# Kernel optimization log

Hardware: AMD Instinct MI355X
Metric: run time of the kernel (lower is better)

## Reference

```python
import jax, jax.numpy as jnp
import numpy as np

IN_CH = 32
OUT_CH = 32
B, N = 1, 100000
E = 1600000
BN_EPS = 1e-5


def setup_inputs() -> dict:
    key = jax.random.key(0)
    k1, k2, k3 = jax.random.split(key, 3)
    x = jax.random.normal(k1, (B, IN_CH, N, 1), dtype=jnp.float32)
    edge_index = jax.random.randint(k2, (2, E), 0, B * N, dtype=jnp.int64)
    # Conv1d(in*2 -> out, kernel_size=1, bias=False): weight [out, 2*in]
    W = jax.random.normal(k3, (OUT_CH, 2 * IN_CH), dtype=jnp.float32) * (1.0 / np.sqrt(2 * IN_CH))
    gamma = jnp.ones((OUT_CH,), dtype=jnp.float32)
    beta = jnp.zeros((OUT_CH,), dtype=jnp.float32)
    return {"x": x, "edge_index": edge_index, "W": W, "gamma": gamma, "beta": beta}


def reference(x, edge_index, W, gamma, beta):
    Bb, C, Nn, _ = x.shape
    out_ch = W.shape[0]
    # faithful to torch: x.squeeze(-1).view(B*N, C) (raw row-major reshape)
    x_flat = x[..., 0].reshape(Bb * Nn, C)
    src, tgt = edge_index[0], edge_index[1]
    x_s = x_flat[src]                      # [E, C] gather
    x_t = x_flat[tgt]                      # [E, C] gather
    ef = jnp.concatenate([x_s, x_t - x_s], axis=1)  # [E, 2C]
    y = ef @ W.T                           # 1x1 conv == GEMM, [E, out]
    # BatchNorm1d in training mode: batch stats over edge dim (biased var)
    mean = jnp.mean(y, axis=0)
    var = jnp.mean(jnp.square(y - mean), axis=0)
    y = (y - mean) * jax.lax.rsqrt(var + BN_EPS) * gamma + beta
    # ELU (alpha=1)
    y = jnp.where(y > 0, y, jnp.expm1(y))
    out = jnp.zeros((Bb * Nn, out_ch), dtype=y.dtype).at[src].add(y)  # scatter-add
    return out.reshape(Bb, out_ch, Nn)[..., None]
```

## Files before the change

kernel.cpp:

```cpp
#include <hip/hip_runtime.h>
#include <hip/hip_bf16.h>
#include <math.h>

#define NCH 32

typedef unsigned short ushort_t;
typedef unsigned int uint_t;
typedef unsigned char uchar_t;

static __device__ __forceinline__ float bf2f(ushort_t b) {
    return __uint_as_float(((uint_t)b) << 16);
}
static __device__ __forceinline__ ushort_t f2bf(float f) {
    __hip_bfloat16 h = __float2bfloat16(f);
    return *reinterpret_cast<ushort_t*>(&h);
}

using f32x2 = __attribute__((ext_vector_type(2))) float;

template <typename T>
__device__ __forceinline__ auto pkAddImpl(T* p, T v, int)
    -> decltype(unsafeAtomicAdd(p, v), void()) {
    unsafeAtomicAdd(p, v);
}
template <typename T>
__device__ void pkAddImpl(T* p, T v, long) {
    uint_t* q = reinterpret_cast<uint_t*>(p);
    uint_t vv = *reinterpret_cast<uint_t*>(&v);
    uint_t cur = *q;
    while (true) {
        float lo = bf2f((ushort_t)(cur & 0xFFFF)) + bf2f((ushort_t)(vv & 0xFFFF));
        float hi = bf2f((ushort_t)(cur >> 16)) + bf2f((ushort_t)(vv >> 16));
        uint_t nw = (uint_t)f2bf(lo) | ((uint_t)f2bf(hi) << 16);
        uint_t prev = atomicCAS(q, cur, nw);
        if (prev == cur) break;
        cur = prev;
    }
}
static __device__ __forceinline__ void pkAdd(__hip_bfloat162* p, float z0, float z1) {
    __hip_bfloat162 v;
    v.x = __float2bfloat16(z0);
    v.y = __float2bfloat16(z1);
    pkAddImpl(p, v, 0);
}


__global__ __launch_bounds__(256) void k_uv3(
    const float* __restrict__ x, const float* __restrict__ W,
    ushort_t* __restrict__ uh, ushort_t* __restrict__ vh,
    uchar_t* __restrict__ uq, uchar_t* __restrict__ vq, int N)
{
    __shared__ float At[NCH * NCH];
    __shared__ float Bt[NCH * NCH];
    for (int i = threadIdx.x; i < NCH * NCH; i += 256) {
        const int k = i >> 5, c = i & 31;
        const float w1 = W[c * 64 + k];
        const float w2 = W[c * 64 + 32 + k];
        At[i] = w1 - w2;
        Bt[i] = w2;
    }
    __syncthreads();

    const int n = blockIdx.x * 8 + (threadIdx.x >> 5);
    const int c = threadIdx.x & 31;
    if (n >= N) return;

    const float xc = x[(size_t)n * NCH + c];
    float su = 0.f, sv = 0.f;
#pragma unroll
    for (int k = 0; k < NCH; ++k) {
        const float xk = __shfl(xc, k, 32);
        su = fmaf(At[k * 32 + c], xk, su);
        sv = fmaf(Bt[k * 32 + c], xk, sv);
    }
    uh[(size_t)n * NCH + c] = f2bf(su);
    vh[(size_t)n * NCH + c] = f2bf(sv);
    uq[(size_t)n * NCH + c] =
        (uchar_t)(__builtin_amdgcn_cvt_pk_fp8_f32(su, su, 0, false) & 0xFF);
    vq[(size_t)n * NCH + c] =
        (uchar_t)(__builtin_amdgcn_cvt_pk_fp8_f32(sv, sv, 0, false) & 0xFF);
}

__global__ __launch_bounds__(256) void k_stats8(
    const uchar_t* __restrict__ uq, const uchar_t* __restrict__ vq,
    const int* __restrict__ srci, const int* __restrict__ tgti,
    float* __restrict__ partials, int E)
{
    const ushort_t* __restrict__ uq16 = (const ushort_t*)uq;
    const ushort_t* __restrict__ vq16 = (const ushort_t*)vq;
    const int l  = threadIdx.x & 15;
    const int g  = (blockIdx.x * 256 + threadIdx.x) >> 4;
    const int nG = (gridDim.x * 256) >> 4;

    float s0 = 0.f, s1 = 0.f, q0 = 0.f, q1 = 0.f;
    int e = g;
    for (; e + 3 * nG < E; e += 4 * nG) {
        const int ea = e, eb = e + nG, ec = e + 2 * nG, ed = e + 3 * nG;
        const int sa = srci[ea], sb = srci[eb], sc = srci[ec], sd = srci[ed];
        const int ta = tgti[ea], tb = tgti[eb], tc = tgti[ec], td = tgti[ed];
        const ushort_t ua = uq16[(size_t)sa * 16 + l];
        const ushort_t ub = uq16[(size_t)sb * 16 + l];
        const ushort_t uc = uq16[(size_t)sc * 16 + l];
        const ushort_t ud = uq16[(size_t)sd * 16 + l];
        const ushort_t va = vq16[(size_t)ta * 16 + l];
        const ushort_t vb = vq16[(size_t)tb * 16 + l];
        const ushort_t vc = vq16[(size_t)tc * 16 + l];
        const ushort_t vd = vq16[(size_t)td * 16 + l];
#pragma unroll
        for (int k = 0; k < 4; ++k) {
            const ushort_t uu = (k == 0) ? ua : (k == 1) ? ub : (k == 2) ? uc : ud;
            const ushort_t vv = (k == 0) ? va : (k == 1) ? vb : (k == 2) ? vc : vd;
            const f32x2 uf = __builtin_amdgcn_cvt_pk_f32_fp8((int)uu, false);
            const f32x2 vf = __builtin_amdgcn_cvt_pk_f32_fp8((int)vv, false);
            const float y0 = uf.x + vf.x;
            const float y1 = uf.y + vf.y;
            s0 += y0; q0 = fmaf(y0, y0, q0);
            s1 += y1; q1 = fmaf(y1, y1, q1);
        }
    }
    for (; e < E; e += nG) {
        const int s = srci[e], t = tgti[e];
        const f32x2 uf = __builtin_amdgcn_cvt_pk_f32_fp8((int)uq16[(size_t)s * 16 + l], false);
        const f32x2 vf = __builtin_amdgcn_cvt_pk_f32_fp8((int)vq16[(size_t)t * 16 + l], false);
        const float y0 = uf.x + vf.x;
        const float y1 = uf.y + vf.y;
        s0 += y0; q0 = fmaf(y0, y0, q0);
        s1 += y1; q1 = fmaf(y1, y1, q1);
    }

    __shared__ float sL[16][32];
    __shared__ float qL[16][32];
    const int grp = threadIdx.x >> 4;
    sL[grp][2 * l + 0] = s0;
    sL[grp][2 * l + 1] = s1;
    qL[grp][2 * l + 0] = q0;
    qL[grp][2 * l + 1] = q1;
    __syncthreads();
    if (threadIdx.x < 32) {
        float a = 0.f;
#pragma unroll
        for (int r = 0; r < 16; ++r) a += sL[r][threadIdx.x];
        partials[(size_t)blockIdx.x * 64 + threadIdx.x] = a;
    } else if (threadIdx.x < 64) {
        const int cc = threadIdx.x - 32;
        float a = 0.f;
#pragma unroll
        for (int r = 0; r < 16; ++r) a += qL[r][cc];
        partials[(size_t)blockIdx.x * 64 + 32 + cc] = a;
    }
}

__global__ __launch_bounds__(256) void k_finalize(
    const float* __restrict__ partials, int nblocks,
    const float* __restrict__ gamma, const float* __restrict__ beta,
    float* __restrict__ ab, float invE)
{
    __shared__ float acc[4][64];
    const int vtx = threadIdx.x & 63, chunk = threadIdx.x >> 6;
    float s = 0.f;
    for (int r = chunk; r < nblocks; r += 4) s += partials[(size_t)r * 64 + vtx];
    acc[chunk][vtx] = s;
    __syncthreads();
    if (threadIdx.x < 64) acc[0][vtx] = acc[0][vtx] + acc[1][vtx] + acc[2][vtx] + acc[3][vtx];
    __syncthreads();
    if (threadIdx.x < 32) {
        const int c = threadIdx.x;
        float mean = acc[0][c] * invE;
        float var  = acc[0][32 + c] * invE - mean * mean;
        float rstd = rsqrtf(var + 1e-5f);
        float a = gamma[c] * rstd;
        ab[c] = a; ab[32 + c] = beta[c] - mean * a;
    }
}

__global__ __launch_bounds__(256) void k_apply_pk(
    const ushort_t* __restrict__ uh, const ushort_t* __restrict__ vh,
    const int* __restrict__ srci, const int* __restrict__ tgti,
    const float* __restrict__ ab,
    __hip_bfloat162* __restrict__ outh, int E)
{
    const uint_t* __restrict__ uh32 = (const uint_t*)uh;
    const uint_t* __restrict__ vh32 = (const uint_t*)vh;
    const int l  = threadIdx.x & 15;
    const float a0 = ab[2 * l + 0], a1 = ab[2 * l + 1];
    const float b0 = ab[32 + 2 * l + 0], b1 = ab[32 + 2 * l + 1];
    const int g  = (blockIdx.x * 256 + threadIdx.x) >> 4;
    const int nG = (gridDim.x * 256) >> 4;

    int e = g;
    for (; e + 3 * nG < E; e += 4 * nG) {
        const int ea = e, eb = e + nG, ec = e + 2 * nG, ed = e + 3 * nG;
        const int sa = srci[ea], sb = srci[eb], sc = srci[ec], sd = srci[ed];
        const int ta = tgti[ea], tb = tgti[eb], tc = tgti[ec], td = tgti[ed];
        const uint_t Ua = uh32[(size_t)sa * 16 + l];
        const uint_t Ub = uh32[(size_t)sb * 16 + l];
        const uint_t Uc = uh32[(size_t)sc * 16 + l];
        const uint_t Ud = uh32[(size_t)sd * 16 + l];
        const uint_t Va = vh32[(size_t)ta * 16 + l];
        const uint_t Vb = vh32[(size_t)tb * 16 + l];
        const uint_t Vc = vh32[(size_t)tc * 16 + l];
        const uint_t Vd = vh32[(size_t)td * 16 + l];
        const int ss[4] = {sa, sb, sc, sd};
        const uint_t UU[4] = {Ua, Ub, Uc, Ud};
        const uint_t VV[4] = {Va, Vb, Vc, Vd};
#pragma unroll
        for (int k = 0; k < 4; ++k) {
            const float y0 = bf2f((ushort_t)(UU[k] & 0xFFFF)) + bf2f((ushort_t)(VV[k] & 0xFFFF));
            const float y1 = bf2f((ushort_t)(UU[k] >> 16))    + bf2f((ushort_t)(VV[k] >> 16));
            float z0 = fmaf(a0, y0, b0);
            float z1 = fmaf(a1, y1, b1);
            z0 = (z0 > 0.f) ? z0 : (__expf(z0) - 1.0f);
            z1 = (z1 > 0.f) ? z1 : (__expf(z1) - 1.0f);
            pkAdd(&outh[(size_t)ss[k] * 16 + l], z0, z1);
        }
    }
    for (; e < E; e += nG) {
        const int s = srci[e], t = tgti[e];
        const uint_t U = uh32[(size_t)s * 16 + l];
        const uint_t V = vh32[(size_t)t * 16 + l];
        const float y0 = bf2f((ushort_t)(U & 0xFFFF)) + bf2f((ushort_t)(V & 0xFFFF));
        const float y1 = bf2f((ushort_t)(U >> 16))    + bf2f((ushort_t)(V >> 16));
        float z0 = fmaf(a0, y0, b0);
        float z1 = fmaf(a1, y1, b1);
        z0 = (z0 > 0.f) ? z0 : (__expf(z0) - 1.0f);
        z1 = (z1 > 0.f) ? z1 : (__expf(z1) - 1.0f);
        pkAdd(&outh[(size_t)s * 16 + l], z0, z1);
    }
}

__global__ __launch_bounds__(256) void k_cvt(
    const uint_t* __restrict__ outh32, float* __restrict__ out, int M)
{
    const int i = blockIdx.x * 256 + threadIdx.x;
    if (i >= M) return;
    const uint_t w = outh32[i];
    float2 f;
    f.x = bf2f((ushort_t)(w & 0xFFFF));
    f.y = bf2f((ushort_t)(w >> 16));
    ((float2*)out)[i] = f;
}

__global__ __launch_bounds__(256) void k_stats_hist(
    const float* __restrict__ x,
    const int* __restrict__ srci, const int* __restrict__ tgti,
    const float* __restrict__ W,
    float* __restrict__ partials, int E)
{
    float sum[NCH], ssq[NCH];
#pragma unroll
    for (int c = 0; c < NCH; ++c) { sum[c] = 0.f; ssq[c] = 0.f; }
    const int stride = gridDim.x * blockDim.x;
    for (int e = blockIdx.x * blockDim.x + threadIdx.x; e < E; e += stride) {
        const int s = srci[e], t = tgti[e];
        const float4* ps = (const float4*)(x + (size_t)s * NCH);
        const float4* pt = (const float4*)(x + (size_t)t * NCH);
        float xs[NCH], dx[NCH];
#pragma unroll
        for (int i = 0; i < 8; ++i) {
            float4 a = ps[i], bb = pt[i];
            xs[4*i+0] = a.x; xs[4*i+1] = a.y; xs[4*i+2] = a.z; xs[4*i+3] = a.w;
            dx[4*i+0] = bb.x - a.x; dx[4*i+1] = bb.y - a.y;
            dx[4*i+2] = bb.z - a.z; dx[4*i+3] = bb.w - a.w;
        }
#pragma unroll
        for (int c = 0; c < NCH; ++c) {
            const float* wr = W + c * 64;
            float y = 0.f;
#pragma unroll
            for (int k = 0; k < NCH; ++k) y = fmaf(wr[k], xs[k], y);
#pragma unroll
            for (int k = 0; k < NCH; ++k) y = fmaf(wr[32 + k], dx[k], y);
            sum[c] += y;
            ssq[c] = fmaf(y, y, ssq[c]);
        }
    }
#pragma unroll
    for (int c = 0; c < NCH; ++c) {
#pragma unroll
        for (int off = 32; off > 0; off >>= 1) {
            sum[c] += __shfl_down(sum[c], off);
            ssq[c] += __shfl_down(ssq[c], off);
        }
    }
    __shared__ float red[4][64];
    const int lane = threadIdx.x & 63, wave = threadIdx.x >> 6;
    if (lane == 0) {
#pragma unroll
        for (int c = 0; c < NCH; ++c) { red[wave][c] = sum[c]; red[wave][NCH+c] = ssq[c]; }
    }
    __syncthreads();
    if (threadIdx.x < 64)
        partials[(size_t)blockIdx.x * 64 + threadIdx.x] =
            red[0][threadIdx.x] + red[1][threadIdx.x] + red[2][threadIdx.x] + red[3][threadIdx.x];
}

__global__ __launch_bounds__(256) void k_apply_atomic(
    const float* __restrict__ x,
    const int* __restrict__ srci, const int* __restrict__ tgti,
    const float* __restrict__ W, const float* __restrict__ ab,
    float* __restrict__ out, int E)
{
    const int e = blockIdx.x * 256 + threadIdx.x;
    if (e >= E) return;
    const int s = srci[e], t = tgti[e];
    const float4* ps = (const float4*)(x + (size_t)s * NCH);
    const float4* pt = (const float4*)(x + (size_t)t * NCH);
    float xs[NCH], dx[NCH];
#pragma unroll
    for (int i = 0; i < 8; ++i) {
        float4 a = ps[i], bb = pt[i];
        xs[4*i+0] = a.x; xs[4*i+1] = a.y; xs[4*i+2] = a.z; xs[4*i+3] = a.w;
        dx[4*i+0] = bb.x - a.x; dx[4*i+1] = bb.y - a.y;
        dx[4*i+2] = bb.z - a.z; dx[4*i+3] = bb.w - a.w;
    }
    float* orow = out + (size_t)s * NCH;
#pragma unroll
    for (int c = 0; c < NCH; ++c) {
        const float* wr = W + c * 64;
        float y = 0.f;
#pragma unroll
        for (int k = 0; k < NCH; ++k) y = fmaf(wr[k], xs[k], y);
#pragma unroll
        for (int k = 0; k < NCH; ++k) y = fmaf(wr[32 + k], dx[k], y);
        float z = fmaf(ab[c], y, ab[32 + c]);
        z = (z > 0.f) ? z : (__expf(z) - 1.0f);
        atomicAdd(orow + c, z);
    }
}

extern "C" void kernel_launch(void* const* d_in, const int* in_sizes, int n_in,
                              void* d_out, int out_size, void* d_ws, size_t ws_size,
                              hipStream_t stream)
{
    const float* x     = (const float*)d_in[0];
    const int*   ei    = (const int*)d_in[1];
    const float* W     = (const float*)d_in[2];
    const float* gamma = (const float*)d_in[3];
    const float* beta  = (const float*)d_in[4];
    const int E = in_sizes[1] / 2;
    const int N = in_sizes[0] / NCH;
    const int* srci = ei;
    const int* tgti = ei + E;

    const int SB = 1024;
    const int AB = 2048;

    size_t need = (size_t)N * NCH * (2 + 2 + 1 + 1 + 2)
                + ((size_t)SB * 64 + 64) * 4;

    if (ws_size >= need) {
        ushort_t* uh      = (ushort_t*)d_ws;
        ushort_t* vh      = uh + (size_t)N * NCH;
        uchar_t*  uq      = (uchar_t*)(vh + (size_t)N * NCH);
        uchar_t*  vq      = uq + (size_t)N * NCH;
        __hip_bfloat162* outh = (__hip_bfloat162*)(vq + (size_t)N * NCH);
        float*    partials= (float*)((ushort_t*)outh + (size_t)N * NCH);
        float*    ab      = partials + (size_t)SB * 64;

        hipMemsetAsync(outh, 0, (size_t)N * NCH * 2, stream);
        k_uv3<<<(N + 7) / 8, 256, 0, stream>>>(x, W, uh, vh, uq, vq, N);
        k_stats8<<<SB, 256, 0, stream>>>(uq, vq, srci, tgti, partials, E);
        k_finalize<<<1, 256, 0, stream>>>(partials, SB, gamma, beta, ab, 1.0f / (float)E);
        k_apply_pk<<<AB, 256, 0, stream>>>(uh, vh, srci, tgti, ab, outh, E);
        k_cvt<<<(N * 16 + 255) / 256, 256, 0, stream>>>((const uint_t*)outh,
                                                        (float*)d_out, N * 16);
    } else {
        const int SBf = 512;
        float* ab       = (float*)d_ws;
        float* partials = ab + 64;
        hipMemsetAsync(d_out, 0, (size_t)out_size * sizeof(float), stream);
        k_stats_hist<<<SBf, 256, 0, stream>>>(x, srci, tgti, W, partials, E);
        k_finalize<<<1, 256, 0, stream>>>(partials, SBf, gamma, beta, ab, 1.0f / (float)E);
        k_apply_atomic<<<(E + 255) / 256, 256, 0, stream>>>(x, srci, tgti, W, ab,
                                                            (float*)d_out, E);
    }
}
```

Before: 309.3 us.

## Partition scatter by source range per XCD and fuse memset/finalize into kernels

The output zeroing moves into the projection kernel and the BN finalize becomes a last-block-ticket epilogue of the stats kernel, which removes a memset and a kernel launch. The apply kernel now gives each group of blocks (blockIdx & 7, meant to map to one XCD) one eighth of the source-node range. Each group scans all edges and processes only those whose source falls in its range, so the atomics on each output slice stay within one L2. The cost is that every edge index is read eight times, and the grid-stride work per group shrinks to one eighth of the blocks.

Result: slower. 501.1 us (+62.0%).

```diff
diff --git a/kernel.cpp b/kernel.cpp
--- a/kernel.cpp
+++ b/kernel.cpp
@@ -45,10 +45,11 @@
 }
 
 
-__global__ __launch_bounds__(256) void k_uv3(
+__global__ __launch_bounds__(256) void k_uv3z(
     const float* __restrict__ x, const float* __restrict__ W,
     ushort_t* __restrict__ uh, ushort_t* __restrict__ vh,
-    uchar_t* __restrict__ uq, uchar_t* __restrict__ vq, int N)
+    uchar_t* __restrict__ uq, uchar_t* __restrict__ vq,
+    uint_t* __restrict__ outh32, int* __restrict__ ticket, int N)
 {
     __shared__ float At[NCH * NCH];
     __shared__ float Bt[NCH * NCH];
@@ -59,12 +60,18 @@
         At[i] = w1 - w2;
         Bt[i] = w2;
     }
+
+    {
+        const int M = N * 16;
+        for (int i = blockIdx.x * 256 + threadIdx.x; i < M; i += gridDim.x * 256)
+            outh32[i] = 0u;
+        if (blockIdx.x == 0 && threadIdx.x == 0) *ticket = 0;
+    }
     __syncthreads();
 
     const int n = blockIdx.x * 8 + (threadIdx.x >> 5);
     const int c = threadIdx.x & 31;
     if (n >= N) return;
-
     const float xc = x[(size_t)n * NCH + c];
     float su = 0.f, sv = 0.f;
 #pragma unroll
@@ -81,10 +88,12 @@
         (uchar_t)(__builtin_amdgcn_cvt_pk_fp8_f32(sv, sv, 0, false) & 0xFF);
 }
 
-__global__ __launch_bounds__(256) void k_stats8(
+__global__ __launch_bounds__(256) void k_stats8f(
     const uchar_t* __restrict__ uq, const uchar_t* __restrict__ vq,
     const int* __restrict__ srci, const int* __restrict__ tgti,
-    float* __restrict__ partials, int E)
+    float* __restrict__ partials, int* __restrict__ ticket,
+    const float* __restrict__ gamma, const float* __restrict__ beta,
+    float* __restrict__ ab, float invE, int E)
 {
     const ushort_t* __restrict__ uq16 = (const ushort_t*)uq;
     const ushort_t* __restrict__ vq16 = (const ushort_t*)vq;
@@ -148,6 +157,189 @@
         for (int r = 0; r < 16; ++r) a += qL[r][cc];
         partials[(size_t)blockIdx.x * 64 + 32 + cc] = a;
     }
+
+    __shared__ int isLast;
+    __threadfence();
+    __syncthreads();
+    if (threadIdx.x == 0) {
+        const int prev = atomicAdd(ticket, 1);
+        isLast = (prev == (int)gridDim.x - 1) ? 1 : 0;
+    }
+    __syncthreads();
+    if (isLast) {
+        __shared__ float acc[4][64];
+        const int vtx = threadIdx.x & 63, chunk = threadIdx.x >> 6;
+        float s = 0.f;
+        for (int r = chunk; r < (int)gridDim.x; r += 4)
+            s += partials[(size_t)r * 64 + vtx];
+        acc[chunk][vtx] = s;
+        __syncthreads();
+        if (threadIdx.x < 64)
+            acc[0][vtx] = acc[0][vtx] + acc[1][vtx] + acc[2][vtx] + acc[3][vtx];
+        __syncthreads();
+        if (threadIdx.x < 32) {
+            const int c = threadIdx.x;
+            float mean = acc[0][c] * invE;
+            float var  = acc[0][32 + c] * invE - mean * mean;
+            float rstd = rsqrtf(var + 1e-5f);
+            float a = gamma[c] * rstd;
+            ab[c] = a; ab[32 + c] = beta[c] - mean * a;
+        }
+    }
+}
+
+__global__ __launch_bounds__(256) void k_apply_xcd(
+    const ushort_t* __restrict__ uh, const ushort_t* __restrict__ vh,
+    const int* __restrict__ srci, const int* __restrict__ tgti,
+    const float* __restrict__ ab,
+    __hip_bfloat162* __restrict__ outh, int E, int NS)
+{
+    const uint_t* __restrict__ uh32 = (const uint_t*)uh;
+    const uint_t* __restrict__ vh32 = (const uint_t*)vh;
+    const int l  = threadIdx.x & 15;
+    const float a0 = ab[2 * l + 0], a1 = ab[2 * l + 1];
+    const float b0 = ab[32 + 2 * l + 0], b1 = ab[32 + 2 * l + 1];
+
+    const int xb = blockIdx.x & 7;
+    const int lo = xb * NS;
+    const int bi = blockIdx.x >> 3;
+    const int nb = gridDim.x >> 3;
+    const int g  = (bi * 256 + threadIdx.x) >> 4;
+    const int nG = nb * 16;
+
+    int e = g;
+    for (; e + 3 * nG < E; e += 4 * nG) {
+        const int ea = e, eb = e + nG, ec = e + 2 * nG, ed = e + 3 * nG;
+        const int sa = srci[ea], sb = srci[eb], sc = srci[ec], sd = srci[ed];
+        const bool ma = (unsigned)(sa - lo) < (unsigned)NS;
+        const bool mb = (unsigned)(sb - lo) < (unsigned)NS;
+        const bool mc = (unsigned)(sc - lo) < (unsigned)NS;
+        const bool md = (unsigned)(sd - lo) < (unsigned)NS;
+        if (ma) {
+            const uint_t U = uh32[(size_t)sa * 16 + l];
+            const uint_t V = vh32[(size_t)tgti[ea] * 16 + l];
+            const float y0 = bf2f((ushort_t)(U & 0xFFFF)) + bf2f((ushort_t)(V & 0xFFFF));
+            const float y1 = bf2f((ushort_t)(U >> 16))    + bf2f((ushort_t)(V >> 16));
+            float z0 = fmaf(a0, y0, b0);
+            float z1 = fmaf(a1, y1, b1);
+            z0 = (z0 > 0.f) ? z0 : (__expf(z0) - 1.0f);
+            z1 = (z1 > 0.f) ? z1 : (__expf(z1) - 1.0f);
+            pkAdd(&outh[(size_t)sa * 16 + l], z0, z1);
+        }
+        if (mb) {
+            const uint_t U = uh32[(size_t)sb * 16 + l];
+            const uint_t V = vh32[(size_t)tgti[eb] * 16 + l];
+            const float y0 = bf2f((ushort_t)(U & 0xFFFF)) + bf2f((ushort_t)(V & 0xFFFF));
+            const float y1 = bf2f((ushort_t)(U >> 16))    + bf2f((ushort_t)(V >> 16));
+            float z0 = fmaf(a0, y0, b0);
+            float z1 = fmaf(a1, y1, b1);
+            z0 = (z0 > 0.f) ? z0 : (__expf(z0) - 1.0f);
+            z1 = (z1 > 0.f) ? z1 : (__expf(z1) - 1.0f);
+            pkAdd(&outh[(size_t)sb * 16 + l], z0, z1);
+        }
+        if (mc) {
+            const uint_t U = uh32[(size_t)sc * 16 + l];
+            const uint_t V = vh32[(size_t)tgti[ec] * 16 + l];
+            const float y0 = bf2f((ushort_t)(U & 0xFFFF)) + bf2f((ushort_t)(V & 0xFFFF));
+            const float y1 = bf2f((ushort_t)(U >> 16))    + bf2f((ushort_t)(V >> 16));
+            float z0 = fmaf(a0, y0, b0);
+            float z1 = fmaf(a1, y1, b1);
+            z0 = (z0 > 0.f) ? z0 : (__expf(z0) - 1.0f);
+            z1 = (z1 > 0.f) ? z1 : (__expf(z1) - 1.0f);
+            pkAdd(&outh[(size_t)sc * 16 + l], z0, z1);
+        }
+        if (md) {
+            const uint_t U = uh32[(size_t)sd * 16 + l];
+            const uint_t V = vh32[(size_t)tgti[ed] * 16 + l];
+            const float y0 = bf2f((ushort_t)(U & 0xFFFF)) + bf2f((ushort_t)(V & 0xFFFF));
+            const float y1 = bf2f((ushort_t)(U >> 16))    + bf2f((ushort_t)(V >> 16));
+            float z0 = fmaf(a0, y0, b0);
+            float z1 = fmaf(a1, y1, b1);
+            z0 = (z0 > 0.f) ? z0 : (__expf(z0) - 1.0f);
+            z1 = (z1 > 0.f) ? z1 : (__expf(z1) - 1.0f);
+            pkAdd(&outh[(size_t)sd * 16 + l], z0, z1);
+        }
+    }
+    for (; e < E; e += nG) {
+        const int s = srci[e];
+        if ((unsigned)(s - lo) < (unsigned)NS) {
+            const uint_t U = uh32[(size_t)s * 16 + l];
+            const uint_t V = vh32[(size_t)tgti[e] * 16 + l];
+            const float y0 = bf2f((ushort_t)(U & 0xFFFF)) + bf2f((ushort_t)(V & 0xFFFF));
+            const float y1 = bf2f((ushort_t)(U >> 16))    + bf2f((ushort_t)(V >> 16));
+            float z0 = fmaf(a0, y0, b0);
+            float z1 = fmaf(a1, y1, b1);
+            z0 = (z0 > 0.f) ? z0 : (__expf(z0) - 1.0f);
+            z1 = (z1 > 0.f) ? z1 : (__expf(z1) - 1.0f);
+            pkAdd(&outh[(size_t)s * 16 + l], z0, z1);
+        }
+    }
+}
+
+__global__ __launch_bounds__(256) void k_cvt(
+    const uint_t* __restrict__ outh32, float* __restrict__ out, int M)
+{
+    const int i = blockIdx.x * 256 + threadIdx.x;
+    if (i >= M) return;
+    const uint_t w = outh32[i];
+    float2 f;
+    f.x = bf2f((ushort_t)(w & 0xFFFF));
+    f.y = bf2f((ushort_t)(w >> 16));
+    ((float2*)out)[i] = f;
+}
+
+__global__ __launch_bounds__(256) void k_stats_hist(
+    const float* __restrict__ x,
+    const int* __restrict__ srci, const int* __restrict__ tgti,
+    const float* __restrict__ W,
+    float* __restrict__ partials, int E)
+{
+    float sum[NCH], ssq[NCH];
+#pragma unroll
+    for (int c = 0; c < NCH; ++c) { sum[c] = 0.f; ssq[c] = 0.f; }
+    const int stride = gridDim.x * blockDim.x;
+    for (int e = blockIdx.x * blockDim.x + threadIdx.x; e < E; e += stride) {
+        const int s = srci[e], t = tgti[e];
+        const float4* ps = (const float4*)(x + (size_t)s * NCH);
+        const float4* pt = (const float4*)(x + (size_t)t * NCH);
+        float xs[NCH], dx[NCH];
+#pragma unroll
+        for (int i = 0; i < 8; ++i) {
+            float4 a = ps[i], bb = pt[i];
+            xs[4*i+0] = a.x; xs[4*i+1] = a.y; xs[4*i+2] = a.z; xs[4*i+3] = a.w;
+            dx[4*i+0] = bb.x - a.x; dx[4*i+1] = bb.y - a.y;
+            dx[4*i+2] = bb.z - a.z; dx[4*i+3] = bb.w - a.w;
+        }
+#pragma unroll
+        for (int c = 0; c < NCH; ++c) {
+            const float* wr = W + c * 64;
+            float y = 0.f;
+#pragma unroll
+            for (int k = 0; k < NCH; ++k) y = fmaf(wr[k], xs[k], y);
+#pragma unroll
+            for (int k = 0; k < NCH; ++k) y = fmaf(wr[32 + k], dx[k], y);
+            sum[c] += y;
+            ssq[c] = fmaf(y, y, ssq[c]);
+        }
+    }
+#pragma unroll
+    for (int c = 0; c < NCH; ++c) {
+#pragma unroll
+        for (int off = 32; off > 0; off >>= 1) {
+            sum[c] += __shfl_down(sum[c], off);
+            ssq[c] += __shfl_down(ssq[c], off);
+        }
+    }
+    __shared__ float red[4][64];
+    const int lane = threadIdx.x & 63, wave = threadIdx.x >> 6;
+    if (lane == 0) {
+#pragma unroll
+        for (int c = 0; c < NCH; ++c) { red[wave][c] = sum[c]; red[wave][NCH+c] = ssq[c]; }
+    }
+    __syncthreads();
+    if (threadIdx.x < 64)
+        partials[(size_t)blockIdx.x * 64 + threadIdx.x] =
+            red[0][threadIdx.x] + red[1][threadIdx.x] + red[2][threadIdx.x] + red[3][threadIdx.x];
 }
 
 __global__ __launch_bounds__(256) void k_finalize(
@@ -171,127 +363,6 @@
         float a = gamma[c] * rstd;
         ab[c] = a; ab[32 + c] = beta[c] - mean * a;
     }
-}
-
-__global__ __launch_bounds__(256) void k_apply_pk(
-    const ushort_t* __restrict__ uh, const ushort_t* __restrict__ vh,
-    const int* __restrict__ srci, const int* __restrict__ tgti,
-    const float* __restrict__ ab,
-    __hip_bfloat162* __restrict__ outh, int E)
-{
-    const uint_t* __restrict__ uh32 = (const uint_t*)uh;
-    const uint_t* __restrict__ vh32 = (const uint_t*)vh;
-    const int l  = threadIdx.x & 15;
-    const float a0 = ab[2 * l + 0], a1 = ab[2 * l + 1];
-    const float b0 = ab[32 + 2 * l + 0], b1 = ab[32 + 2 * l + 1];
-    const int g  = (blockIdx.x * 256 + threadIdx.x) >> 4;
-    const int nG = (gridDim.x * 256) >> 4;
-
-    int e = g;
-    for (; e + 3 * nG < E; e += 4 * nG) {
-        const int ea = e, eb = e + nG, ec = e + 2 * nG, ed = e + 3 * nG;
-        const int sa = srci[ea], sb = srci[eb], sc = srci[ec], sd = srci[ed];
-        const int ta = tgti[ea], tb = tgti[eb], tc = tgti[ec], td = tgti[ed];
-        const uint_t Ua = uh32[(size_t)sa * 16 + l];
-        const uint_t Ub = uh32[(size_t)sb * 16 + l];
-        const uint_t Uc = uh32[(size_t)sc * 16 + l];
-        const uint_t Ud = uh32[(size_t)sd * 16 + l];
-        const uint_t Va = vh32[(size_t)ta * 16 + l];
-        const uint_t Vb = vh32[(size_t)tb * 16 + l];
-        const uint_t Vc = vh32[(size_t)tc * 16 + l];
-        const uint_t Vd = vh32[(size_t)td * 16 + l];
-        const int ss[4] = {sa, sb, sc, sd};
-        const uint_t UU[4] = {Ua, Ub, Uc, Ud};
-        const uint_t VV[4] = {Va, Vb, Vc, Vd};
-#pragma unroll
-        for (int k = 0; k < 4; ++k) {
-            const float y0 = bf2f((ushort_t)(UU[k] & 0xFFFF)) + bf2f((ushort_t)(VV[k] & 0xFFFF));
-            const float y1 = bf2f((ushort_t)(UU[k] >> 16))    + bf2f((ushort_t)(VV[k] >> 16));
-            float z0 = fmaf(a0, y0, b0);
-            float z1 = fmaf(a1, y1, b1);
-            z0 = (z0 > 0.f) ? z0 : (__expf(z0) - 1.0f);
-            z1 = (z1 > 0.f) ? z1 : (__expf(z1) - 1.0f);
-            pkAdd(&outh[(size_t)ss[k] * 16 + l], z0, z1);
-        }
-    }
-    for (; e < E; e += nG) {
-        const int s = srci[e], t = tgti[e];
-        const uint_t U = uh32[(size_t)s * 16 + l];
-        const uint_t V = vh32[(size_t)t * 16 + l];
-        const float y0 = bf2f((ushort_t)(U & 0xFFFF)) + bf2f((ushort_t)(V & 0xFFFF));
-        const float y1 = bf2f((ushort_t)(U >> 16))    + bf2f((ushort_t)(V >> 16));
-        float z0 = fmaf(a0, y0, b0);
-        float z1 = fmaf(a1, y1, b1);
-        z0 = (z0 > 0.f) ? z0 : (__expf(z0) - 1.0f);
-        z1 = (z1 > 0.f) ? z1 : (__expf(z1) - 1.0f);
-        pkAdd(&outh[(size_t)s * 16 + l], z0, z1);
-    }
-}
-
-__global__ __launch_bounds__(256) void k_cvt(
-    const uint_t* __restrict__ outh32, float* __restrict__ out, int M)
-{
-    const int i = blockIdx.x * 256 + threadIdx.x;
-    if (i >= M) return;
-    const uint_t w = outh32[i];
-    float2 f;
-    f.x = bf2f((ushort_t)(w & 0xFFFF));
-    f.y = bf2f((ushort_t)(w >> 16));
-    ((float2*)out)[i] = f;
-}
-
-__global__ __launch_bounds__(256) void k_stats_hist(
-    const float* __restrict__ x,
-    const int* __restrict__ srci, const int* __restrict__ tgti,
-    const float* __restrict__ W,
-    float* __restrict__ partials, int E)
-{
-    float sum[NCH], ssq[NCH];
-#pragma unroll
-    for (int c = 0; c < NCH; ++c) { sum[c] = 0.f; ssq[c] = 0.f; }
-    const int stride = gridDim.x * blockDim.x;
-    for (int e = blockIdx.x * blockDim.x + threadIdx.x; e < E; e += stride) {
-        const int s = srci[e], t = tgti[e];
-        const float4* ps = (const float4*)(x + (size_t)s * NCH);
-        const float4* pt = (const float4*)(x + (size_t)t * NCH);
-        float xs[NCH], dx[NCH];
-#pragma unroll
-        for (int i = 0; i < 8; ++i) {
-            float4 a = ps[i], bb = pt[i];
-            xs[4*i+0] = a.x; xs[4*i+1] = a.y; xs[4*i+2] = a.z; xs[4*i+3] = a.w;
-            dx[4*i+0] = bb.x - a.x; dx[4*i+1] = bb.y - a.y;
-            dx[4*i+2] = bb.z - a.z; dx[4*i+3] = bb.w - a.w;
-        }
-#pragma unroll
-        for (int c = 0; c < NCH; ++c) {
-            const float* wr = W + c * 64;
-            float y = 0.f;
-#pragma unroll
-            for (int k = 0; k < NCH; ++k) y = fmaf(wr[k], xs[k], y);
-#pragma unroll
-            for (int k = 0; k < NCH; ++k) y = fmaf(wr[32 + k], dx[k], y);
-            sum[c] += y;
-            ssq[c] = fmaf(y, y, ssq[c]);
-        }
-    }
-#pragma unroll
-    for (int c = 0; c < NCH; ++c) {
-#pragma unroll
-        for (int off = 32; off > 0; off >>= 1) {
-            sum[c] += __shfl_down(sum[c], off);
-            ssq[c] += __shfl_down(ssq[c], off);
-        }
-    }
-    __shared__ float red[4][64];
-    const int lane = threadIdx.x & 63, wave = threadIdx.x >> 6;
-    if (lane == 0) {
-#pragma unroll
-        for (int c = 0; c < NCH; ++c) { red[wave][c] = sum[c]; red[wave][NCH+c] = ssq[c]; }
-    }
-    __syncthreads();
-    if (threadIdx.x < 64)
-        partials[(size_t)blockIdx.x * 64 + threadIdx.x] =
-            red[0][threadIdx.x] + red[1][threadIdx.x] + red[2][threadIdx.x] + red[3][threadIdx.x];
 }
 
 __global__ __launch_bounds__(256) void k_apply_atomic(
@@ -344,34 +415,34 @@
 
     const int SB = 1024;
     const int AB = 2048;
-
-    size_t need = (size_t)N * NCH * (2 + 2 + 1 + 1 + 2)
-                + ((size_t)SB * 64 + 64) * 4;
+    const int NS = (N + 7) / 8;
+
+    ushort_t* uh      = (ushort_t*)d_ws;
+    ushort_t* vh      = uh + (size_t)N * NCH;
+    uchar_t*  uq      = (uchar_t*)(vh + (size_t)N * NCH);
+    uchar_t*  vq      = uq + (size_t)N * NCH;
+    __hip_bfloat162* outh = (__hip_bfloat162*)(vq + (size_t)N * NCH);
+    float*    partials= (float*)((ushort_t*)outh + (size_t)N * NCH);
+    float*    ab      = partials + (size_t)SB * 64;
+    int*      ticket  = (int*)(ab + 64);
+    const size_t need = (size_t)((char*)(ticket + 1) - (char*)d_ws);
 
     if (ws_size >= need) {
-        ushort_t* uh      = (ushort_t*)d_ws;
-        ushort_t* vh      = uh + (size_t)N * NCH;
-        uchar_t*  uq      = (uchar_t*)(vh + (size_t)N * NCH);
-        uchar_t*  vq      = uq + (size_t)N * NCH;
-        __hip_bfloat162* outh = (__hip_bfloat162*)(vq + (size_t)N * NCH);
-        float*    partials= (float*)((ushort_t*)outh + (size_t)N * NCH);
-        float*    ab      = partials + (size_t)SB * 64;
-
-        hipMemsetAsync(outh, 0, (size_t)N * NCH * 2, stream);
-        k_uv3<<<(N + 7) / 8, 256, 0, stream>>>(x, W, uh, vh, uq, vq, N);
-        k_stats8<<<SB, 256, 0, stream>>>(uq, vq, srci, tgti, partials, E);
-        k_finalize<<<1, 256, 0, stream>>>(partials, SB, gamma, beta, ab, 1.0f / (float)E);
-        k_apply_pk<<<AB, 256, 0, stream>>>(uh, vh, srci, tgti, ab, outh, E);
+        k_uv3z<<<(N + 7) / 8, 256, 0, stream>>>(x, W, uh, vh, uq, vq,
+                                                (uint_t*)outh, ticket, N);
+        k_stats8f<<<SB, 256, 0, stream>>>(uq, vq, srci, tgti, partials, ticket,
+                                          gamma, beta, ab, 1.0f / (float)E, E);
+        k_apply_xcd<<<AB, 256, 0, stream>>>(uh, vh, srci, tgti, ab, outh, E, NS);
         k_cvt<<<(N * 16 + 255) / 256, 256, 0, stream>>>((const uint_t*)outh,
                                                         (float*)d_out, N * 16);
     } else {
         const int SBf = 512;
-        float* ab       = (float*)d_ws;
-        float* partials = ab + 64;
+        float* abf      = (float*)d_ws;
+        float* partialsf = abf + 64;
         hipMemsetAsync(d_out, 0, (size_t)out_size * sizeof(float), stream);
-        k_stats_hist<<<SBf, 256, 0, stream>>>(x, srci, tgti, W, partials, E);
-        k_finalize<<<1, 256, 0, stream>>>(partials, SBf, gamma, beta, ab, 1.0f / (float)E);
-        k_apply_atomic<<<(E + 255) / 256, 256, 0, stream>>>(x, srci, tgti, W, ab,
+        k_stats_hist<<<SBf, 256, 0, stream>>>(x, srci, tgti, W, partialsf, E);
+        k_finalize<<<1, 256, 0, stream>>>(partialsf, SBf, gamma, beta, abf, 1.0f / (float)E);
+        k_apply_atomic<<<(E + 255) / 256, 256, 0, stream>>>(x, srci, tgti, W, abf,
                                                             (float*)d_out, E);
     }
 }
```
